# Optimization experiments

Hardware: AMD Instinct MI355X
Metric: run time of the kernel (lower is better)

Reference implementation:

```python
import jax, jax.numpy as jnp
import numpy as np

NEG = -1e30  # log-domain "zero" (safe in fp32/bf16 logaddexp)
EPS = 1e-7   # keras backend epsilon used by K.ctc_batch_cost


def setup_inputs() -> dict:
    key = jax.random.key(0)
    k1, k2 = jax.random.split(key)
    B, T, C, L = 64, 1024, 512, 128
    y_pred = jax.random.uniform(k1, (B, T, C), dtype=jnp.float32)
    y_true = jax.random.randint(k2, (B, L), 0, C - 1)  # blank = C-1 excluded
    return {"y_true": y_true, "y_pred": y_pred}


def ctc_batch_cost(y_true, y_pred):
    """Faithful jax port of keras.backend.ctc_batch_cost with full-length
    labels/inputs (as the CTCLayer passes input_length=T, label_length=L
    for every batch element). Returns per-example loss of shape [B, 1].

    K.ctc_batch_cost computes log(y_pred + eps) and feeds it to
    tf.nn.ctc_loss, which applies an internal softmax; we replicate that
    with log_softmax(log(y_pred + eps)). blank index = C - 1.
    """
    B, T, C = y_pred.shape
    L = y_true.shape[1]
    blank = C - 1
    logp = jax.nn.log_softmax(jnp.log(y_pred + EPS), axis=-1)  # [B,T,C]

    # Extended label sequence with interleaved blanks: length S = 2L+1
    S = 2 * L + 1
    ext = jnp.full((B, S), blank, dtype=y_true.dtype).at[:, 1::2].set(y_true)
    ext_m2 = jnp.concatenate(
        [jnp.full((B, 2), -1, dtype=ext.dtype), ext[:, :-2]], axis=1)
    # alpha[s-2] -> alpha[s] skip allowed iff ext[s] != blank and ext[s] != ext[s-2]
    skip = (ext != blank) & (ext != ext_m2)  # [B,S]

    # Emission log-probs gathered along the extended sequence: [B,T,S]
    emit = jnp.take_along_axis(
        logp, jnp.broadcast_to(ext[:, None, :], (B, T, S)), axis=2)

    # alpha_0: only states 0 (blank) and 1 (first label) are reachable
    alpha0 = (jnp.full((B, S), NEG, dtype=logp.dtype)
              .at[:, 0].set(emit[:, 0, 0])
              .at[:, 1].set(emit[:, 0, 1]))

    neg1 = jnp.full((B, 1), NEG, dtype=logp.dtype)
    neg2 = jnp.full((B, 2), NEG, dtype=logp.dtype)

    def step(alpha, emit_t):
        a1 = jnp.concatenate([neg1, alpha[:, :-1]], axis=1)   # stay->next
        a2 = jnp.concatenate([neg2, alpha[:, :-2]], axis=1)   # skip blank
        a2 = jnp.where(skip, a2, NEG)
        comb = jnp.logaddexp(jnp.logaddexp(alpha, a1), a2)
        return comb + emit_t, None

    emit_tm = jnp.transpose(emit, (1, 0, 2))  # time-major [T,B,S]
    alphaT, _ = jax.lax.scan(step, alpha0, emit_tm[1:])

    # p(labels) = alpha_T[S-1] + alpha_T[S-2]
    loss = -jnp.logaddexp(alphaT[:, -1], alphaT[:, -2])  # [B]
    return loss[:, None]


def reference(y_true, y_pred):
    return ctc_batch_cost(y_true, y_pred)
```

## Files before the change

### kernel.cpp

```cpp
#include <hip/hip_runtime.h>


#define EPSF 1e-7f
static constexpr int NB = 64;
static constexpr int NT = 1024;
static constexpr int NC = 512;
static constexpr int NL = 128;
static constexpr int CHUNK = 32;
static constexpr int NCH = NT / CHUNK;

typedef unsigned int uint32;
typedef unsigned short ushort16;

__device__ __forceinline__ ushort16 rn_bf16(float x) {
    uint32 b = __float_as_uint(x);
    return (ushort16)((b + 0x7FFFu + ((b >> 16) & 1u)) >> 16);
}

__global__ __launch_bounds__(256) void ctc_prep(const float* __restrict__ Y,
                                                const int* __restrict__ y_true,
                                                uint32* __restrict__ elab,
                                                float* __restrict__ eblank,
                                                int mode) {
    int gtid = blockIdx.x * 256 + threadIdx.x;
    int w = gtid >> 6;
    int lane = gtid & 63;
    int b = w >> 10;
    const float* row = Y + (size_t)w * NC;

    float4 v0 = *reinterpret_cast<const float4*>(row + lane * 4);
    float4 v1 = *reinterpret_cast<const float4*>(row + (NC / 2) + lane * 4);
    float s = ((v0.x + v0.y) + (v0.z + v0.w)) + ((v1.x + v1.y) + (v1.z + v1.w));
#pragma unroll
    for (int d = 1; d < 64; d <<= 1) s += __shfl_xor(s, d);
    float inv = 256.0f / (s + NC * EPSF);

    if (mode == 1) {
        int2 lp = *reinterpret_cast<const int2*>(y_true + b * NL + lane * 2);
        float ex = (row[lp.x] + EPSF) * inv;
        float ey = (row[lp.y] + EPSF) * inv;
        uint32 pk = (uint32)rn_bf16(ex) | ((uint32)rn_bf16(ey) << 16);
        elab[(size_t)w * (NL / 2) + lane] = pk;
        if (lane == 0) eblank[w] = (row[NC - 1] + EPSF) * inv;
    } else {
        if (lane == 0) eblank[w] = inv;
    }
}

__device__ __forceinline__ float dpp_wave_shr1(float x) {
    return __int_as_float(__builtin_amdgcn_update_dpp(
        0, __float_as_int(x), 0x138, 0xF, 0xF, true));
}

__device__ __forceinline__ float dpp_wave_max(float m) {
#define DPPMAX_(ctrl)                                                     \
    m = fmaxf(m, __int_as_float(__builtin_amdgcn_update_dpp(              \
                     0, __float_as_int(m), ctrl, 0xF, 0xF, true)))
    DPPMAX_(0x111);
    DPPMAX_(0x112);
    DPPMAX_(0x114);
    DPPMAX_(0x118);
    DPPMAX_(0x142);
    DPPMAX_(0x143);
#undef DPPMAX_
    return __int_as_float(
        __builtin_amdgcn_readlane(__float_as_int(m), 63));
}

__global__ __launch_bounds__(64) void ctc_rec1(const uint32* __restrict__ A,
                                               const float* __restrict__ Bv,
                                               const int* __restrict__ y_true,
                                               float* __restrict__ out) {
    const int b = blockIdx.x;
    const int l = threadIdx.x;
    const int* lab = y_true + b * NL;

    int lab_m1 = (l == 0) ? -1 : lab[2 * l - 1];
    int lab0 = lab[2 * l];
    int lab1 = lab[2 * l + 1];
    float sk0 = (lab0 != lab_m1) ? 1.0f : 0.0f;
    float sk1 = (lab1 != lab0) ? 1.0f : 0.0f;

    float p0 = (l == 0) ? 1.0f : 0.0f;
    float p1 = 0.0f, p2 = 0.0f, p3 = 0.0f, pS = 0.0f;
    int ksum = 0;

    uint32 L0[CHUNK], L1[CHUNK];
    float E0[CHUNK], E1[CHUNK];

    auto load = [&](int c, uint32(&L)[CHUNK], float(&E)[CHUNK]) {
        const uint32* base = A + ((size_t)b * NT + c * CHUNK) * (NL / 2) + l;
#pragma unroll
        for (int j = 0; j < CHUNK; j++) L[j] = base[(size_t)j * (NL / 2)];
        const float* eb = Bv + b * NT + c * CHUNK;
#pragma unroll
        for (int q = 0; q < CHUNK / 4; q++)
            *reinterpret_cast<float4*>(&E[4 * q]) =
                *reinterpret_cast<const float4*>(eb + 4 * q);
    };

    auto process = [&](uint32(&L)[CHUNK], float(&E)[CHUNK]) {
#pragma unroll
        for (int j = 0; j < CHUNK; j++) {
            float eb = E[j];
            float ex = __uint_as_float(L[j] << 16);
            float ey = __uint_as_float(L[j] & 0xFFFF0000u);
            float s3 = dpp_wave_shr1(p3);
            float n0 = (p0 + s3) * eb;
            float n1 = (p1 + p0 + sk0 * s3) * ex;
            float n2 = (p2 + p1) * eb;
            float n3 = (p3 + p2 + sk1 * p1) * ey;
            pS = (pS + p3) * eb;
            p0 = n0; p1 = n1; p2 = n2; p3 = n3;

            if ((j & 15) == 15) {
                float m = fmaxf(fmaxf(p0, p1), fmaxf(p2, p3));
                m = fmaxf(m, (l == 63) ? pS : 0.0f);
                float mall = fmaxf(dpp_wave_max(m), 1e-30f);
                int e = (int)(__float_as_uint(mall) >> 23) - 127;
                float sc = __uint_as_float((uint32)(127 - e) << 23);
                p0 *= sc; p1 *= sc; p2 *= sc; p3 *= sc; pS *= sc;
                ksum += e;
            }
        }
    };

    load(0, L0, E0);
    for (int c = 0; c < NCH; c += 2) {
        if (c + 1 < NCH) load(c + 1, L1, E1);
        process(L0, E0);
        if (c + 2 < NCH) load(c + 2, L0, E0);
        process(L1, E1);
    }

    if (l == 63) {
        float tot = p3 + pS;
        out[b] = -(logf(tot) +
                   (float)(ksum - 8192) * 0.69314718055994531f);
    }
}

__global__ __launch_bounds__(64) void ctc_rec0(const float* __restrict__ A,
                                               const float* __restrict__ Bv,
                                               const int* __restrict__ y_true,
                                               float* __restrict__ out) {
    const int b = blockIdx.x;
    const int l = threadIdx.x;
    const int* lab = y_true + b * NL;

    int lab_m1 = (l == 0) ? -1 : lab[2 * l - 1];
    int lab0 = lab[2 * l];
    int lab1 = lab[2 * l + 1];
    float sk0 = (lab0 != lab_m1) ? 1.0f : 0.0f;
    float sk1 = (lab1 != lab0) ? 1.0f : 0.0f;

    float p0 = (l == 0) ? 1.0f : 0.0f;
    float p1 = 0.0f, p2 = 0.0f, p3 = 0.0f, pS = 0.0f;
    int ksum = 0;

    for (int t = 0; t < NT; t++) {
        const float* base = A + ((size_t)b * NT + t) * NC;
        float iv = Bv[b * NT + t];
        float eb = (base[NC - 1] + EPSF) * iv;
        float ex = (base[lab0] + EPSF) * iv;
        float ey = (base[lab1] + EPSF) * iv;
        float s3 = dpp_wave_shr1(p3);
        float n0 = (p0 + s3) * eb;
        float n1 = (p1 + p0 + sk0 * s3) * ex;
        float n2 = (p2 + p1) * eb;
        float n3 = (p3 + p2 + sk1 * p1) * ey;
        pS = (pS + p3) * eb;
        p0 = n0; p1 = n1; p2 = n2; p3 = n3;
        if ((t & 15) == 15) {
            float m = fmaxf(fmaxf(p0, p1), fmaxf(p2, p3));
            m = fmaxf(m, (l == 63) ? pS : 0.0f);
            float mall = fmaxf(dpp_wave_max(m), 1e-30f);
            int e = (int)(__float_as_uint(mall) >> 23) - 127;
            float sc = __uint_as_float((uint32)(127 - e) << 23);
            p0 *= sc; p1 *= sc; p2 *= sc; p3 *= sc; pS *= sc;
            ksum += e;
        }
    }

    if (l == 63) {
        float tot = p3 + pS;
        out[b] = -(logf(tot) +
                   (float)(ksum - 8192) * 0.69314718055994531f);
    }
}

extern "C" void kernel_launch(void* const* d_in, const int* in_sizes, int n_in,
                              void* d_out, int out_size, void* d_ws, size_t ws_size,
                              hipStream_t stream) {
    const int* y_true = (const int*)d_in[0];
    const float* y_pred = (const float*)d_in[1];
    float* out = (float*)d_out;

    const size_t elab_bytes = (size_t)NB * NT * (NL / 2) * sizeof(uint32);
    const size_t eb_bytes = (size_t)NB * NT * sizeof(float);

    if (ws_size >= elab_bytes + eb_bytes) {
        uint32* elab = (uint32*)d_ws;
        float* eblank = (float*)((char*)d_ws + elab_bytes);
        ctc_prep<<<NB * NT / 4, 256, 0, stream>>>(y_pred, y_true, elab, eblank, 1);
        ctc_rec1<<<NB, 64, 0, stream>>>(elab, eblank, y_true, out);
    } else {
        float* invb = (float*)d_ws;
        ctc_prep<<<NB * NT / 4, 256, 0, stream>>>(y_pred, y_true, nullptr, invb, 0);
        ctc_rec0<<<NB, 64, 0, stream>>>(y_pred, invb, y_true, out);
    }
}
```

Before: 64.63 us.

## Normalize emissions by blank probability to drop per-step blank multiplies

The prep kernel now stores each label emission divided by the blank emission, so the recurrence only multiplies the label states and skips the blank multiply at every step. The factored-out per-timestep blank probability is applied once as a sum of logs, computed in parallel up front. The chunk size drops to 16, with rescaling once per chunk, and prefetch deepens to four register buffers. This shortens the serial dependency chain in the latency-bound recurrence, at some risk of range and precision trouble because the ratios can be large.

```diff
diff --git a/kernel.cpp b/kernel.cpp
--- a/kernel.cpp
+++ b/kernel.cpp
@@ -6,20 +6,19 @@
 static constexpr int NT = 1024;
 static constexpr int NC = 512;
 static constexpr int NL = 128;
-static constexpr int CHUNK = 32;
+static constexpr int CHUNK = 16;
 static constexpr int NCH = NT / CHUNK;
 
 typedef unsigned int uint32;
-typedef unsigned short ushort16;
-
-__device__ __forceinline__ ushort16 rn_bf16(float x) {
+
+__device__ __forceinline__ unsigned short rn_bf16(float x) {
     uint32 b = __float_as_uint(x);
-    return (ushort16)((b + 0x7FFFu + ((b >> 16) & 1u)) >> 16);
+    return (unsigned short)((b + 0x7FFFu + ((b >> 16) & 1u)) >> 16);
 }
 
 __global__ __launch_bounds__(256) void ctc_prep(const float* __restrict__ Y,
                                                 const int* __restrict__ y_true,
-                                                uint32* __restrict__ elab,
+                                                uint32* __restrict__ qlab,
                                                 float* __restrict__ eblank,
                                                 int mode) {
     int gtid = blockIdx.x * 256 + threadIdx.x;
@@ -33,17 +32,19 @@
     float s = ((v0.x + v0.y) + (v0.z + v0.w)) + ((v1.x + v1.y) + (v1.z + v1.w));
 #pragma unroll
     for (int d = 1; d < 64; d <<= 1) s += __shfl_xor(s, d);
-    float inv = 256.0f / (s + NC * EPSF);
 
     if (mode == 1) {
+        float rb = row[NC - 1] + EPSF;
+        float inv = 1.0f / (s + NC * EPSF);
+        float rbi = 1.0f / rb;
         int2 lp = *reinterpret_cast<const int2*>(y_true + b * NL + lane * 2);
-        float ex = (row[lp.x] + EPSF) * inv;
-        float ey = (row[lp.y] + EPSF) * inv;
-        uint32 pk = (uint32)rn_bf16(ex) | ((uint32)rn_bf16(ey) << 16);
-        elab[(size_t)w * (NL / 2) + lane] = pk;
-        if (lane == 0) eblank[w] = (row[NC - 1] + EPSF) * inv;
+        float qx = (row[lp.x] + EPSF) * rbi;
+        float qy = (row[lp.y] + EPSF) * rbi;
+        uint32 pk = (uint32)rn_bf16(qx) | ((uint32)rn_bf16(qy) << 16);
+        qlab[(size_t)w * (NL / 2) + lane] = pk;
+        if (lane == 0) eblank[w] = rb * inv;
     } else {
-        if (lane == 0) eblank[w] = inv;
+        if (lane == 0) eblank[w] = 256.0f / (s + NC * EPSF);
     }
 }
 
@@ -56,15 +57,21 @@
 #define DPPMAX_(ctrl)                                                     \
     m = fmaxf(m, __int_as_float(__builtin_amdgcn_update_dpp(              \
                      0, __float_as_int(m), ctrl, 0xF, 0xF, true)))
-    DPPMAX_(0x111);
-    DPPMAX_(0x112);
-    DPPMAX_(0x114);
-    DPPMAX_(0x118);
-    DPPMAX_(0x142);
-    DPPMAX_(0x143);
+    DPPMAX_(0x111); DPPMAX_(0x112); DPPMAX_(0x114); DPPMAX_(0x118);
+    DPPMAX_(0x142); DPPMAX_(0x143);
 #undef DPPMAX_
     return __int_as_float(
         __builtin_amdgcn_readlane(__float_as_int(m), 63));
+}
+
+__device__ __forceinline__ float dpp_wave_sum63(float v) {
+#define DPPADD_(ctrl)                                                     \
+    v += __int_as_float(__builtin_amdgcn_update_dpp(                      \
+        0, __float_as_int(v), ctrl, 0xF, 0xF, true))
+    DPPADD_(0x111); DPPADD_(0x112); DPPADD_(0x114); DPPADD_(0x118);
+    DPPADD_(0x142); DPPADD_(0x143);
+#undef DPPADD_
+    return v;
 }
 
 __global__ __launch_bounds__(64) void ctc_rec1(const uint32* __restrict__ A,
@@ -81,62 +88,63 @@
     float sk0 = (lab0 != lab_m1) ? 1.0f : 0.0f;
     float sk1 = (lab1 != lab0) ? 1.0f : 0.0f;
 
+    float slog = 0.0f;
+#pragma unroll
+    for (int k = 0; k < NT / 64; k++)
+        slog += logf(Bv[b * NT + k * 64 + l]);
+    float sred = dpp_wave_sum63(slog);
+
     float p0 = (l == 0) ? 1.0f : 0.0f;
     float p1 = 0.0f, p2 = 0.0f, p3 = 0.0f, pS = 0.0f;
     int ksum = 0;
 
-    uint32 L0[CHUNK], L1[CHUNK];
-    float E0[CHUNK], E1[CHUNK];
-
-    auto load = [&](int c, uint32(&L)[CHUNK], float(&E)[CHUNK]) {
+    uint32 L0[CHUNK], L1[CHUNK], L2[CHUNK], L3[CHUNK];
+
+    auto load = [&](int c, uint32(&L)[CHUNK]) {
         const uint32* base = A + ((size_t)b * NT + c * CHUNK) * (NL / 2) + l;
 #pragma unroll
         for (int j = 0; j < CHUNK; j++) L[j] = base[(size_t)j * (NL / 2)];
-        const float* eb = Bv + b * NT + c * CHUNK;
-#pragma unroll
-        for (int q = 0; q < CHUNK / 4; q++)
-            *reinterpret_cast<float4*>(&E[4 * q]) =
-                *reinterpret_cast<const float4*>(eb + 4 * q);
     };
 
-    auto process = [&](uint32(&L)[CHUNK], float(&E)[CHUNK]) {
+    auto process = [&](uint32(&L)[CHUNK]) {
 #pragma unroll
         for (int j = 0; j < CHUNK; j++) {
-            float eb = E[j];
-            float ex = __uint_as_float(L[j] << 16);
-            float ey = __uint_as_float(L[j] & 0xFFFF0000u);
+            float qx = __uint_as_float(L[j] << 16);
+            float qy = __uint_as_float(L[j] & 0xFFFF0000u);
             float s3 = dpp_wave_shr1(p3);
-            float n0 = (p0 + s3) * eb;
-            float n1 = (p1 + p0 + sk0 * s3) * ex;
-            float n2 = (p2 + p1) * eb;
-            float n3 = (p3 + p2 + sk1 * p1) * ey;
-            pS = (pS + p3) * eb;
+            float n0 = p0 + s3;
+            float n1 = (p1 + p0 + sk0 * s3) * qx;
+            float n2 = p2 + p1;
+            float n3 = (p3 + p2 + sk1 * p1) * qy;
+            pS = pS + p3;
             p0 = n0; p1 = n1; p2 = n2; p3 = n3;
-
-            if ((j & 15) == 15) {
-                float m = fmaxf(fmaxf(p0, p1), fmaxf(p2, p3));
-                m = fmaxf(m, (l == 63) ? pS : 0.0f);
-                float mall = fmaxf(dpp_wave_max(m), 1e-30f);
-                int e = (int)(__float_as_uint(mall) >> 23) - 127;
-                float sc = __uint_as_float((uint32)(127 - e) << 23);
-                p0 *= sc; p1 *= sc; p2 *= sc; p3 *= sc; pS *= sc;
-                ksum += e;
-            }
         }
+        float m = fmaxf(fmaxf(p0, p1), fmaxf(p2, p3));
+        m = fmaxf(m, (l == 63) ? pS : 0.0f);
+        float mall = fmaxf(dpp_wave_max(m), 1e-30f);
+        int e = (int)(__float_as_uint(mall) >> 23) - 127;
+        float sc = __uint_as_float((uint32)(127 - e) << 23);
+        p0 *= sc; p1 *= sc; p2 *= sc; p3 *= sc; pS *= sc;
+        ksum += e;
     };
 
-    load(0, L0, E0);
-    for (int c = 0; c < NCH; c += 2) {
-        if (c + 1 < NCH) load(c + 1, L1, E1);
-        process(L0, E0);
-        if (c + 2 < NCH) load(c + 2, L0, E0);
-        process(L1, E1);
+    load(0, L0);
+    load(1, L1);
+    load(2, L2);
+    for (int c = 0; c < NCH; c += 4) {
+        if (c + 3 < NCH) load(c + 3, L3);
+        process(L0);
+        if (c + 4 < NCH) load(c + 4, L0);
+        process(L1);
+        if (c + 5 < NCH) load(c + 5, L1);
+        process(L2);
+        if (c + 6 < NCH) load(c + 6, L2);
+        process(L3);
     }
 
     if (l == 63) {
         float tot = p3 + pS;
-        out[b] = -(logf(tot) +
-                   (float)(ksum - 8192) * 0.69314718055994531f);
+        out[b] = -(logf(tot) + (float)ksum * 0.69314718055994531f + sred);
     }
 }
 
@@ -196,14 +204,14 @@
     const float* y_pred = (const float*)d_in[1];
     float* out = (float*)d_out;
 
-    const size_t elab_bytes = (size_t)NB * NT * (NL / 2) * sizeof(uint32);
+    const size_t qlab_bytes = (size_t)NB * NT * (NL / 2) * sizeof(uint32);
     const size_t eb_bytes = (size_t)NB * NT * sizeof(float);
 
-    if (ws_size >= elab_bytes + eb_bytes) {
-        uint32* elab = (uint32*)d_ws;
-        float* eblank = (float*)((char*)d_ws + elab_bytes);
-        ctc_prep<<<NB * NT / 4, 256, 0, stream>>>(y_pred, y_true, elab, eblank, 1);
-        ctc_rec1<<<NB, 64, 0, stream>>>(elab, eblank, y_true, out);
+    if (ws_size >= qlab_bytes + eb_bytes) {
+        uint32* qlab = (uint32*)d_ws;
+        float* eblank = (float*)((char*)d_ws + qlab_bytes);
+        ctc_prep<<<NB * NT / 4, 256, 0, stream>>>(y_pred, y_true, qlab, eblank, 1);
+        ctc_rec1<<<NB, 64, 0, stream>>>(qlab, eblank, y_true, out);
     } else {
         float* invb = (float*)d_ws;
         ctc_prep<<<NB * NT / 4, 256, 0, stream>>>(y_pred, y_true, nullptr, invb, 0);
```

After: 65.80 us. About the same (+1.8%).
